# Optimization experiments

Measured on AMD Instinct MI355X. Metric: run time of the kernel, lower is better.

The kernel has to match this reference:

```python
import jax, jax.numpy as jnp
import numpy as np

B, S, D, H = 4, 1024, 1024, 16
DH = D // H  # head dim = 64
PAD = -1e7   # padding_num in source
EPS = 1e-3   # keras LayerNormalization default epsilon


def setup_inputs() -> dict:
    key = jax.random.key(0)
    ks = jax.random.split(key, 8)
    return {
        "queries": jax.random.normal(ks[0], (B, S, D), jnp.float32),
        "keys": jax.random.normal(ks[1], (B, S, D), jnp.float32),
        "values": jax.random.normal(ks[2], (B, S, D), jnp.float32),
        "query_masks": jax.random.randint(ks[3], (B, S), 0, 2, jnp.int32),
        "key_masks": jax.random.randint(ks[4], (B, S), 0, 2, jnp.int32),
        "Wq": jax.random.normal(ks[5], (D, D), jnp.float32) * (D ** -0.5),
        "Wk": jax.random.normal(ks[6], (D, D), jnp.float32) * (D ** -0.5),
        "Wv": jax.random.normal(ks[7], (D, D), jnp.float32) * (D ** -0.5),
        "gamma": jnp.ones((D,), jnp.float32),
        "beta": jnp.zeros((D,), jnp.float32),
    }


def reference(queries, keys, values, query_masks, key_masks, Wq, Wk, Wv, gamma, beta):
    # QKV projections (no bias)
    Q = queries @ Wq  # [B,S,D]
    K = keys @ Wk
    V = values @ Wv
    # split heads: tf.split(axis=2)+concat(axis=0) == head-major layout [H,B,S,DH]
    Qh = Q.reshape(B, S, H, DH).transpose(2, 0, 1, 3)
    Kh = K.reshape(B, S, H, DH).transpose(2, 0, 1, 3)
    Vh = V.reshape(B, S, H, DH).transpose(2, 0, 1, 3)
    # scaled scores; note source scales by head_dim ** 0.5 (d_k of split K)
    scores = jnp.einsum("hbqd,hbkd->hbqk", Qh, Kh) / (DH ** 0.5)
    # additive key mask: positions where key_mask==0 get large negative
    scores = jnp.where(key_masks[None, :, None, :] == 0, PAD, scores)
    attn = jax.nn.softmax(scores, axis=-1)
    # multiplicative query mask AFTER softmax (as in source)
    attn = attn * query_masks[None, :, :, None].astype(jnp.float32)
    out = jnp.einsum("hbqk,hbkd->hbqd", attn, Vh)  # [H,B,S,DH]
    # merge heads back: concat over feature axis in head order
    out = out.transpose(1, 2, 0, 3).reshape(B, S, D)
    # residual + LayerNorm
    res = queries + out
    mean = jnp.mean(res, axis=-1, keepdims=True)
    var = jnp.mean(jnp.square(res - mean), axis=-1, keepdims=True)
    return gamma * (res - mean) * jax.lax.rsqrt(var + EPS) + beta
```

## Files before the change

### kernel.cpp

```cpp
#include <hip/hip_runtime.h>

#define BB   4
#define SS   1024
#define DD   1024
#define HH   16
#define DHH  64
#define LN_EPS  (1e-3f)
#define NTT  ((size_t)BB * SS * DD)

typedef unsigned short u16;
typedef __attribute__((ext_vector_type(8))) short bf16x8;
typedef __attribute__((ext_vector_type(4))) float f32x4;

__device__ __forceinline__ u16 f2bf(float f) {
    union { float f; unsigned int u; } v; v.f = f;
    return (u16)((v.u + 0x7FFFu + ((v.u >> 16) & 1u)) >> 16);
}

__device__ __forceinline__ void cp16(void* lds, const void* g) {
    __builtin_amdgcn_global_load_lds(
        (const __attribute__((address_space(1))) unsigned int*)g,
        (__attribute__((address_space(3))) unsigned int*)lds, 16, 0, 0);
}


__device__ __forceinline__ void phase_conv(const float* __restrict__ q,
                                           const float* __restrict__ k,
                                           const float* __restrict__ v,
                                           u16* __restrict__ Abf,
                                           int gtid, int nthr) {
    const int total = (int)(3 * NTT / 8);
    for (int i = gtid; i < total; i += nthr) {
        const float* s = (i < 524288) ? q : (i < 1048576) ? k : v;
        const int off = i & 524287;
        const float4 f0 = ((const float4*)s)[off * 2];
        const float4 f1 = ((const float4*)s)[off * 2 + 1];
        union { u16 u[8]; uint4 o; } t;
        t.u[0] = f2bf(f0.x); t.u[1] = f2bf(f0.y);
        t.u[2] = f2bf(f0.z); t.u[3] = f2bf(f0.w);
        t.u[4] = f2bf(f1.x); t.u[5] = f2bf(f1.y);
        t.u[6] = f2bf(f1.z); t.u[7] = f2bf(f1.w);
        ((uint4*)Abf)[i] = t.o;
    }
}

__device__ __forceinline__ void phase_wtile(float (*Ts)[65], int vb,
                                            const float* __restrict__ Wq,
                                            const float* __restrict__ Wk,
                                            const float* __restrict__ Wv,
                                            u16* __restrict__ WtA) {
    const int tid = threadIdx.x;
    const float* W = (vb < 256) ? Wq : (vb < 512) ? Wk : Wv;
    u16* Wt = WtA + (size_t)(vb >> 8) * DD * DD;
    const int idx = vb & 255;
    const int k0 = (idx >> 4) * 64, n0 = (idx & 15) * 64;
    #pragma unroll
    for (int it = 0; it < 4; ++it) {
        const int i2 = tid + it * 256;
        const int r = i2 >> 4, c4 = (i2 & 15) * 4;
        const float4 vv = *(const float4*)&W[(size_t)(k0 + r) * DD + n0 + c4];
        Ts[r][c4 + 0] = vv.x; Ts[r][c4 + 1] = vv.y;
        Ts[r][c4 + 2] = vv.z; Ts[r][c4 + 3] = vv.w;
    }
    __syncthreads();
    const int n = tid >> 2, kc = (tid & 3) * 16;
    #pragma unroll
    for (int p = 0; p < 8; ++p) {
        const unsigned int lo = f2bf(Ts[kc + p * 2 + 0][n]);
        const unsigned int hi = f2bf(Ts[kc + p * 2 + 1][n]);
        *(unsigned int*)&Wt[(size_t)(n0 + n) * DD + k0 + kc + p * 2] = lo | (hi << 16);
    }
}

template <int NJ>
__device__ __forceinline__ void gemm_tile(u16* __restrict__ smem,
                                          const u16* __restrict__ A,
                                          const u16* __restrict__ B,
                                          int m0, int n0, int z,
                                          u16* __restrict__ Qbf,
                                          u16* __restrict__ Kbf,
                                          u16* __restrict__ Vtb) {
    u16* As = smem;
    u16* Bs = smem + 8192;
    const int tid  = threadIdx.x;
    const int wave = tid >> 6, lane = tid & 63;
    const int ln = lane & 15, quad = lane >> 4;
    const int mw = (wave & 1) * 64, nw = (wave >> 1) * (NJ * 16);

    f32x4 acc[4][NJ];
    #pragma unroll
    for (int i = 0; i < 4; ++i)
        #pragma unroll
        for (int j = 0; j < NJ; ++j) acc[i][j] = (f32x4){0.f, 0.f, 0.f, 0.f};

    for (int k0 = 0; k0 < DD; k0 += 64) {
        __syncthreads();
        #pragma unroll
        for (int w = 0; w < 4; ++w) {
            const int s = w * 256 + wave * 64 + lane;
            const int r = s >> 3, csrc = (s & 7) ^ (r & 7);
            cp16(&As[(size_t)(w * 256 + wave * 64) * 8],
                 &A[(size_t)(m0 + r) * DD + k0 + csrc * 8]);
        }
        #pragma unroll
        for (int w = 0; w < NJ; ++w) {
            const int s = w * 256 + wave * 64 + lane;
            const int r = s >> 3, csrc = (s & 7) ^ (r & 7);
            cp16(&Bs[(size_t)(w * 256 + wave * 64) * 8],
                 &B[(size_t)(n0 + r) * DD + k0 + csrc * 8]);
        }
        __syncthreads();

        #pragma unroll
        for (int kk = 0; kk < 2; ++kk) {
            bf16x8 af[4], bfv[NJ];
            #pragma unroll
            for (int i = 0; i < 4; ++i) {
                const int r = mw + i * 16 + ln;
                af[i] = *(const bf16x8*)&As[((r << 3) + ((kk * 4 + quad) ^ (r & 7))) << 3];
            }
            #pragma unroll
            for (int j = 0; j < NJ; ++j) {
                const int r = nw + j * 16 + ln;
                bfv[j] = *(const bf16x8*)&Bs[((r << 3) + ((kk * 4 + quad) ^ (r & 7))) << 3];
            }
            #pragma unroll
            for (int i = 0; i < 4; ++i)
                #pragma unroll
                for (int j = 0; j < NJ; ++j)
                    acc[i][j] = __builtin_amdgcn_mfma_f32_16x16x32_bf16(af[i], bfv[j], acc[i][j], 0, 0, 0);
        }
    }

    if (z < 2) {
        u16* C = (z == 0) ? Qbf : Kbf;
        const float scale = (z == 0) ? 0.125f : 1.0f;
        #pragma unroll
        for (int i = 0; i < 4; ++i) {
            const int mbase = m0 + mw + i * 16 + quad * 4;
            const int bb = mbase >> 10, sb = mbase & 1023;
            #pragma unroll
            for (int j = 0; j < NJ; ++j) {
                const int n = n0 + nw + j * 16 + ln;
                const int hh = n >> 6, dh = n & 63;
                #pragma unroll
                for (int r = 0; r < 4; ++r)
                    C[(((size_t)bb * HH + hh) * SS + sb + r) * DHH + dh] =
                        f2bf(acc[i][j][r] * scale);
            }
        }
    } else {
        #pragma unroll
        for (int i = 0; i < 4; ++i) {
            const int mbase = m0 + mw + i * 16 + quad * 4;
            const int bb = mbase >> 10, sb = mbase & 1023;
            #pragma unroll
            for (int j = 0; j < NJ; ++j) {
                const int n = n0 + nw + j * 16 + ln;
                const int hh = n >> 6, dh = n & 63;
                uint2 pk;
                pk.x = (unsigned int)f2bf(acc[i][j][0]) | ((unsigned int)f2bf(acc[i][j][1]) << 16);
                pk.y = (unsigned int)f2bf(acc[i][j][2]) | ((unsigned int)f2bf(acc[i][j][3]) << 16);
                *(uint2*)&Vtb[(((size_t)bb * HH + hh) * DHH + dh) * SS + sb] = pk;
            }
        }
    }
}

__device__ __forceinline__ void phase_gemm(u16* __restrict__ smem, int vb,
                                           const u16* __restrict__ Abf,
                                           const u16* __restrict__ WtA,
                                           u16* __restrict__ Qbf,
                                           u16* __restrict__ Kbf,
                                           u16* __restrict__ Vtb) {
    const int z = (vb < 256) ? 0 : (vb < 512) ? 1 : 2;
    const int xcd = vb & 7;
    const u16* A = Abf + (size_t)z * NTT;
    const u16* B = WtA + (size_t)z * DD * DD;
    if (z < 2) {
        const int t = (vb & 255) >> 3;
        gemm_tile<4>(smem, A, B, (xcd * 4 + (t & 3)) * 128, (t >> 2) * 128,
                     z, Qbf, Kbf, Vtb);
    } else {
        const int t = (vb - 512) >> 3;
        gemm_tile<2>(smem, A, B, (xcd * 4 + (t & 3)) * 128, (t >> 2) * 64,
                     z, Qbf, Kbf, Vtb);
    }
}

__device__ __forceinline__ void phase_attn(u16* __restrict__ smem, int vb,
                                           const u16* __restrict__ Qbf,
                                           const u16* __restrict__ Kbf,
                                           const u16* __restrict__ Vtb,
                                           const int* __restrict__ qmask,
                                           const int* __restrict__ kmask,
                                           float* __restrict__ Ob) {
    u16* QPs = smem;
    u16* Ks  = smem + 4352;
    u16* Vs  = smem + 8448;
    const int tid  = threadIdx.x;
    const int wave = tid >> 6, lane = tid & 63;
    const int ln = lane & 15, quad = lane >> 4;
    const int xcd  = vb & 7;
    const int rest = vb >> 3;
    const int bh   = (rest & 7) * 8 + xcd;
    const int qt   = rest >> 3;
    const int b    = bh >> 4, h = bh & 15;
    const int q0   = qt * 64;
    const size_t bhs = (size_t)b * HH + h;

    #pragma unroll
    for (int w = 0; w < 2; ++w) {
        const int s = w * 256 + wave * 64 + lane;
        const int r = s >> 3, csrc = (s & 7) ^ (r & 7);
        cp16(&QPs[(size_t)(w * 256 + wave * 64) * 8],
             &Qbf[(bhs * SS + q0 + r) * DHH + csrc * 8]);
    }
    __syncthreads();

    bf16x8 qf[2];
    #pragma unroll
    for (int kk = 0; kk < 2; ++kk) {
        const int r = wave * 16 + ln;
        qf[kk] = *(const bf16x8*)&QPs[((r << 3) + ((kk * 4 + quad) ^ (r & 7))) << 3];
    }

    f32x4 o[4] = {};
    float lsum[4] = {0.f, 0.f, 0.f, 0.f};
    const f32x4 zero = {0.f, 0.f, 0.f, 0.f};

    for (int kt = 0; kt < SS / 64; ++kt) {
        __syncthreads();
        #pragma unroll
        for (int w = 0; w < 2; ++w) {
            const int s = w * 256 + wave * 64 + lane;
            const int r = s >> 3, csrc = (s & 7) ^ (r & 7);
            cp16(&Ks[(size_t)(w * 256 + wave * 64) * 8],
                 &Kbf[(bhs * SS + kt * 64 + r) * DHH + csrc * 8]);
            cp16(&Vs[(size_t)(w * 256 + wave * 64) * 8],
                 &Vtb[(bhs * DHH + r) * SS + kt * 64 + csrc * 8]);
        }
        __syncthreads();

        #pragma unroll
        for (int nt = 0; nt < 4; ++nt) {
            const int krow = nt * 16 + ln;
            const bf16x8 k0f = *(const bf16x8*)&Ks[((krow << 3) + ((0 + quad) ^ (krow & 7))) << 3];
            const bf16x8 k1f = *(const bf16x8*)&Ks[((krow << 3) + ((4 + quad) ^ (krow & 7))) << 3];
            f32x4 sacc = __builtin_amdgcn_mfma_f32_16x16x32_bf16(qf[0], k0f, zero, 0, 0, 0);
            sacc = __builtin_amdgcn_mfma_f32_16x16x32_bf16(qf[1], k1f, sacc, 0, 0, 0);
            const int km = kmask[b * SS + kt * 64 + krow];
            #pragma unroll
            for (int r = 0; r < 4; ++r) {
                const float p = km ? __expf(sacc[r]) : 0.0f;
                lsum[r] += p;
                QPs[(wave * 16 + quad * 4 + r) * 68 + nt * 16 + ln] = f2bf(p);
            }
        }

        #pragma unroll
        for (int kk2 = 0; kk2 < 2; ++kk2) {
            const bf16x8 pf = *(const bf16x8*)&QPs[(wave * 16 + ln) * 68 + kk2 * 32 + quad * 8];
            #pragma unroll
            for (int nt2 = 0; nt2 < 4; ++nt2) {
                const int vrow = nt2 * 16 + ln;
                const bf16x8 vf = *(const bf16x8*)&Vs[((vrow << 3) + ((kk2 * 4 + quad) ^ (vrow & 7))) << 3];
                o[nt2] = __builtin_amdgcn_mfma_f32_16x16x32_bf16(pf, vf, o[nt2], 0, 0, 0);
            }
        }
    }

    #pragma unroll
    for (int r = 0; r < 4; ++r) {
        #pragma unroll
        for (int off = 1; off < 16; off <<= 1)
            lsum[r] += __shfl_xor(lsum[r], off);
        const int qq = q0 + wave * 16 + quad * 4 + r;
        const float scale = (float)qmask[b * SS + qq] / lsum[r];
        #pragma unroll
        for (int nt2 = 0; nt2 < 4; ++nt2)
            Ob[((size_t)b * SS + qq) * DD + h * DHH + nt2 * 16 + ln] = o[nt2][r] * scale;
    }
}

__device__ __forceinline__ void phase_ln(int row, float* __restrict__ sred,
                                         const float* __restrict__ q,
                                         const float* __restrict__ Ob,
                                         const float* __restrict__ gamma,
                                         const float* __restrict__ beta,
                                         float* __restrict__ out) {
    const int tid = threadIdx.x;
    const int wid = tid >> 6, lane = tid & 63;
    const float4 qv = ((const float4*)q)[(size_t)row * 256 + tid];
    const float4 av = ((const float4*)Ob)[(size_t)row * 256 + tid];
    float4 vv;
    vv.x = qv.x + av.x; vv.y = qv.y + av.y;
    vv.z = qv.z + av.z; vv.w = qv.w + av.w;

    float sum = vv.x + vv.y + vv.z + vv.w;
    #pragma unroll
    for (int off = 32; off; off >>= 1) sum += __shfl_down(sum, off);
    if (lane == 0) sred[wid] = sum;
    __syncthreads();
    const float mean = (sred[0] + sred[1] + sred[2] + sred[3]) * (1.0f / DD);
    __syncthreads();

    const float dx = vv.x - mean, dy = vv.y - mean;
    const float dz = vv.z - mean, dw = vv.w - mean;
    float vs = dx * dx + dy * dy + dz * dz + dw * dw;
    #pragma unroll
    for (int off = 32; off; off >>= 1) vs += __shfl_down(vs, off);
    if (lane == 0) sred[wid] = vs;
    __syncthreads();
    const float var = (sred[0] + sred[1] + sred[2] + sred[3]) * (1.0f / DD);
    const float inv = rsqrtf(var + LN_EPS);

    const float4 g  = ((const float4*)gamma)[tid];
    const float4 bt = ((const float4*)beta)[tid];
    float4 ov;
    ov.x = g.x * dx * inv + bt.x; ov.y = g.y * dy * inv + bt.y;
    ov.z = g.z * dz * inv + bt.z; ov.w = g.w * dw * inv + bt.w;
    ((float4*)out)[(size_t)row * 256 + tid] = ov;
    __syncthreads();
}

__global__ __launch_bounds__(256) void k_prep(
    const float* __restrict__ q, const float* __restrict__ k,
    const float* __restrict__ v,
    const float* __restrict__ Wq, const float* __restrict__ Wk,
    const float* __restrict__ Wv,
    u16* __restrict__ Abf, u16* __restrict__ WtA) {
    __shared__ float Ts[64][65];
    if (blockIdx.x < 768) phase_wtile(Ts, blockIdx.x, Wq, Wk, Wv, WtA);
    phase_conv(q, k, v, Abf, blockIdx.x * 256 + threadIdx.x, gridDim.x * 256);
}

__global__ __launch_bounds__(256, 4) void k_gemm(
    const u16* __restrict__ Abf, const u16* __restrict__ WtA,
    u16* __restrict__ Qbf, u16* __restrict__ Kbf, u16* __restrict__ Vtb) {
    __shared__ __align__(16) u16 smem[16384];
    phase_gemm(smem, blockIdx.x, Abf, WtA, Qbf, Kbf, Vtb);
}

__global__ __launch_bounds__(256, 4) void k_attn(
    const u16* __restrict__ Qbf, const u16* __restrict__ Kbf,
    const u16* __restrict__ Vtb,
    const int* __restrict__ qmask, const int* __restrict__ kmask,
    float* __restrict__ Ob) {
    __shared__ __align__(16) u16 smem[12544];
    phase_attn(smem, blockIdx.x, Qbf, Kbf, Vtb, qmask, kmask, Ob);
}

__global__ __launch_bounds__(256) void k_ln(
    const float* __restrict__ q, const float* __restrict__ Ob,
    const float* __restrict__ gamma, const float* __restrict__ beta,
    float* __restrict__ out) {
    __shared__ float sred[4];
    #pragma unroll
    for (int rr = 0; rr < 4; ++rr)
        phase_ln(blockIdx.x * 4 + rr, sred, q, Ob, gamma, beta, out);
}

extern "C" void kernel_launch(void* const* d_in, const int* in_sizes, int n_in,
                              void* d_out, int out_size, void* d_ws, size_t ws_size,
                              hipStream_t stream) {
    const float* queries = (const float*)d_in[0];
    const float* keys    = (const float*)d_in[1];
    const float* values  = (const float*)d_in[2];
    const int*   qmask   = (const int*)d_in[3];
    const int*   kmask   = (const int*)d_in[4];
    const float* Wq      = (const float*)d_in[5];
    const float* Wk      = (const float*)d_in[6];
    const float* Wv      = (const float*)d_in[7];
    const float* gamma   = (const float*)d_in[8];
    const float* beta    = (const float*)d_in[9];
    float* out = (float*)d_out;
    u16* ws = (u16*)d_ws;

    u16*   Abf = ws;
    float* Ob  = (float*)ws;
    u16*   Qbf = ws + 3 * NTT;
    u16*   Kbf = Qbf + NTT;
    u16*   Vtb = Kbf + NTT;
    u16*   WtA = Vtb + NTT;

    k_prep<<<1024, 256, 0, stream>>>(queries, keys, values, Wq, Wk, Wv, Abf, WtA);
    k_gemm<<<1024, 256, 0, stream>>>(Abf, WtA, Qbf, Kbf, Vtb);
    k_attn<<<1024, 256, 0, stream>>>(Qbf, Kbf, Vtb, qmask, kmask, Ob);
    k_ln<<<1024, 256, 0, stream>>>(queries, Ob, gamma, beta, out);
}
```

Baseline: 207.4 us.

## Fuse fp32-to-bf16 conversion into GEMM loads and merge LayerNorm into attention

Drops the separate activation conversion pass. The GEMM now reads fp32 q/k/v directly, converts to bf16 in registers and stores to LDS, replacing the async global-to-LDS copy. Weight transposition moves into the GEMM kernel behind a grid-wide atomic flag barrier, and LayerNorm is folded into the attention kernel using per-row-group counters that wait for all 16 heads. This removes two launches and the bf16 activation round trip through memory. The cost is spin-wait barriers that depend on all 1024 blocks being co-resident, which risks deadlock, plus an extra memset and synchronous fp32 loads in the GEMM loop.

```diff
diff --git a/kernel.cpp b/kernel.cpp
--- a/kernel.cpp
+++ b/kernel.cpp
@@ -21,27 +21,6 @@
     __builtin_amdgcn_global_load_lds(
         (const __attribute__((address_space(1))) unsigned int*)g,
         (__attribute__((address_space(3))) unsigned int*)lds, 16, 0, 0);
-}
-
-
-__device__ __forceinline__ void phase_conv(const float* __restrict__ q,
-                                           const float* __restrict__ k,
-                                           const float* __restrict__ v,
-                                           u16* __restrict__ Abf,
-                                           int gtid, int nthr) {
-    const int total = (int)(3 * NTT / 8);
-    for (int i = gtid; i < total; i += nthr) {
-        const float* s = (i < 524288) ? q : (i < 1048576) ? k : v;
-        const int off = i & 524287;
-        const float4 f0 = ((const float4*)s)[off * 2];
-        const float4 f1 = ((const float4*)s)[off * 2 + 1];
-        union { u16 u[8]; uint4 o; } t;
-        t.u[0] = f2bf(f0.x); t.u[1] = f2bf(f0.y);
-        t.u[2] = f2bf(f0.z); t.u[3] = f2bf(f0.w);
-        t.u[4] = f2bf(f1.x); t.u[5] = f2bf(f1.y);
-        t.u[6] = f2bf(f1.z); t.u[7] = f2bf(f1.w);
-        ((uint4*)Abf)[i] = t.o;
-    }
 }
 
 __device__ __forceinline__ void phase_wtile(float (*Ts)[65], int vb,
@@ -74,7 +53,7 @@
 
 template <int NJ>
 __device__ __forceinline__ void gemm_tile(u16* __restrict__ smem,
-                                          const u16* __restrict__ A,
+                                          const float* __restrict__ A,
                                           const u16* __restrict__ B,
                                           int m0, int n0, int z,
                                           u16* __restrict__ Qbf,
@@ -97,10 +76,16 @@
         __syncthreads();
         #pragma unroll
         for (int w = 0; w < 4; ++w) {
-            const int s = w * 256 + wave * 64 + lane;
+            const int s = w * 256 + tid;
             const int r = s >> 3, csrc = (s & 7) ^ (r & 7);
-            cp16(&As[(size_t)(w * 256 + wave * 64) * 8],
-                 &A[(size_t)(m0 + r) * DD + k0 + csrc * 8]);
+            const float4 f0 = *(const float4*)&A[(size_t)(m0 + r) * DD + k0 + csrc * 8];
+            const float4 f1 = *(const float4*)&A[(size_t)(m0 + r) * DD + k0 + csrc * 8 + 4];
+            union { u16 u[8]; uint4 o; } t;
+            t.u[0] = f2bf(f0.x); t.u[1] = f2bf(f0.y);
+            t.u[2] = f2bf(f0.z); t.u[3] = f2bf(f0.w);
+            t.u[4] = f2bf(f1.x); t.u[5] = f2bf(f1.y);
+            t.u[6] = f2bf(f1.z); t.u[7] = f2bf(f1.w);
+            *(uint4*)&As[(size_t)s * 8] = t.o;
         }
         #pragma unroll
         for (int w = 0; w < NJ; ++w) {
@@ -164,27 +149,6 @@
                 *(uint2*)&Vtb[(((size_t)bb * HH + hh) * DHH + dh) * SS + sb] = pk;
             }
         }
-    }
-}
-
-__device__ __forceinline__ void phase_gemm(u16* __restrict__ smem, int vb,
-                                           const u16* __restrict__ Abf,
-                                           const u16* __restrict__ WtA,
-                                           u16* __restrict__ Qbf,
-                                           u16* __restrict__ Kbf,
-                                           u16* __restrict__ Vtb) {
-    const int z = (vb < 256) ? 0 : (vb < 512) ? 1 : 2;
-    const int xcd = vb & 7;
-    const u16* A = Abf + (size_t)z * NTT;
-    const u16* B = WtA + (size_t)z * DD * DD;
-    if (z < 2) {
-        const int t = (vb & 255) >> 3;
-        gemm_tile<4>(smem, A, B, (xcd * 4 + (t & 3)) * 128, (t >> 2) * 128,
-                     z, Qbf, Kbf, Vtb);
-    } else {
-        const int t = (vb - 512) >> 3;
-        gemm_tile<2>(smem, A, B, (xcd * 4 + (t & 3)) * 128, (t >> 2) * 64,
-                     z, Qbf, Kbf, Vtb);
     }
 }
 
@@ -324,41 +288,77 @@
     __syncthreads();
 }
 
-__global__ __launch_bounds__(256) void k_prep(
+__global__ __launch_bounds__(256, 4) void k_gemm(
     const float* __restrict__ q, const float* __restrict__ k,
     const float* __restrict__ v,
     const float* __restrict__ Wq, const float* __restrict__ Wk,
     const float* __restrict__ Wv,
-    u16* __restrict__ Abf, u16* __restrict__ WtA) {
-    __shared__ float Ts[64][65];
-    if (blockIdx.x < 768) phase_wtile(Ts, blockIdx.x, Wq, Wk, Wv, WtA);
-    phase_conv(q, k, v, Abf, blockIdx.x * 256 + threadIdx.x, gridDim.x * 256);
-}
-
-__global__ __launch_bounds__(256, 4) void k_gemm(
-    const u16* __restrict__ Abf, const u16* __restrict__ WtA,
-    u16* __restrict__ Qbf, u16* __restrict__ Kbf, u16* __restrict__ Vtb) {
+    u16* __restrict__ WtA, u16* __restrict__ Qbf, u16* __restrict__ Kbf,
+    u16* __restrict__ Vtb, int* __restrict__ flag) {
     __shared__ __align__(16) u16 smem[16384];
-    phase_gemm(smem, blockIdx.x, Abf, WtA, Qbf, Kbf, Vtb);
+    const int bid = blockIdx.x, tid = threadIdx.x;
+
+    if (bid < 768)
+        phase_wtile((float (*)[65])smem, bid, Wq, Wk, Wv, WtA);
+    __syncthreads();
+    if (tid == 0) {
+        if (bid < 768) {
+            __threadfence();
+            __hip_atomic_fetch_add(flag, 1, __ATOMIC_ACQ_REL, __HIP_MEMORY_SCOPE_AGENT);
+        }
+        while (__hip_atomic_load(flag, __ATOMIC_ACQUIRE, __HIP_MEMORY_SCOPE_AGENT) < 768) {}
+        __threadfence();
+    }
+    __syncthreads();
+
+    const int z = (bid < 256) ? 0 : (bid < 512) ? 1 : 2;
+    const int xcd = bid & 7;
+    const float* A = (z == 0) ? q : (z == 1) ? k : v;
+    const u16* B = WtA + (size_t)z * DD * DD;
+    if (z < 2) {
+        const int t = (bid & 255) >> 3;
+        gemm_tile<4>(smem, A, B, (xcd * 4 + (t & 3)) * 128, (t >> 2) * 128,
+                     z, Qbf, Kbf, Vtb);
+    } else {
+        const int t = (bid - 512) >> 3;
+        gemm_tile<2>(smem, A, B, (xcd * 4 + (t & 3)) * 128, (t >> 2) * 64,
+                     z, Qbf, Kbf, Vtb);
+    }
 }
 
 __global__ __launch_bounds__(256, 4) void k_attn(
     const u16* __restrict__ Qbf, const u16* __restrict__ Kbf,
     const u16* __restrict__ Vtb,
     const int* __restrict__ qmask, const int* __restrict__ kmask,
-    float* __restrict__ Ob) {
+    const float* __restrict__ q, const float* __restrict__ gamma,
+    const float* __restrict__ beta,
+    float* __restrict__ Ob, float* __restrict__ out, int* __restrict__ cnt) {
     __shared__ __align__(16) u16 smem[12544];
-    phase_attn(smem, blockIdx.x, Qbf, Kbf, Vtb, qmask, kmask, Ob);
-}
-
-__global__ __launch_bounds__(256) void k_ln(
-    const float* __restrict__ q, const float* __restrict__ Ob,
-    const float* __restrict__ gamma, const float* __restrict__ beta,
-    float* __restrict__ out) {
-    __shared__ float sred[4];
+    const int bid = blockIdx.x, tid = threadIdx.x;
+
+    phase_attn(smem, bid, Qbf, Kbf, Vtb, qmask, kmask, Ob);
+
+    const int xcd  = bid & 7;
+    const int rest = bid >> 3;
+    const int bh   = (rest & 7) * 8 + xcd;
+    const int qt   = rest >> 3;
+    const int b    = bh >> 4, h = bh & 15;
+    const int gi   = b * 16 + qt;
+
+    __syncthreads();
+    if (tid == 0) {
+        __threadfence();
+        __hip_atomic_fetch_add(&cnt[gi * 16], 1, __ATOMIC_ACQ_REL, __HIP_MEMORY_SCOPE_AGENT);
+        while (__hip_atomic_load(&cnt[gi * 16], __ATOMIC_ACQUIRE, __HIP_MEMORY_SCOPE_AGENT) < 16) {}
+        __threadfence();
+    }
+    __syncthreads();
+
+    float* sred = (float*)smem;
+    const int row0 = b * SS + qt * 64 + h * 4;
     #pragma unroll
     for (int rr = 0; rr < 4; ++rr)
-        phase_ln(blockIdx.x * 4 + rr, sred, q, Ob, gamma, beta, out);
+        phase_ln(row0 + rr, sred, q, Ob, gamma, beta, out);
 }
 
 extern "C" void kernel_launch(void* const* d_in, const int* in_sizes, int n_in,
@@ -377,15 +377,19 @@
     float* out = (float*)d_out;
     u16* ws = (u16*)d_ws;
 
-    u16*   Abf = ws;
     float* Ob  = (float*)ws;
-    u16*   Qbf = ws + 3 * NTT;
+    u16*   Qbf = ws + 2 * NTT;
     u16*   Kbf = Qbf + NTT;
     u16*   Vtb = Kbf + NTT;
     u16*   WtA = Vtb + NTT;
-
-    k_prep<<<1024, 256, 0, stream>>>(queries, keys, values, Wq, Wk, Wv, Abf, WtA);
-    k_gemm<<<1024, 256, 0, stream>>>(Abf, WtA, Qbf, Kbf, Vtb);
-    k_attn<<<1024, 256, 0, stream>>>(Qbf, Kbf, Vtb, qmask, kmask, Ob);
-    k_ln<<<1024, 256, 0, stream>>>(queries, Ob, gamma, beta, out);
-}
+    int*   flags = (int*)(WtA + 3 * (size_t)DD * DD);
+    int*   gflag = flags;
+    int*   cnt   = flags + 16;
+
+    (void)hipMemsetAsync(flags, 0, 8192, stream);
+
+    k_gemm<<<1024, 256, 0, stream>>>(queries, keys, values, Wq, Wk, Wv,
+                                     WtA, Qbf, Kbf, Vtb, gflag);
+    k_attn<<<1024, 256, 0, stream>>>(Qbf, Kbf, Vtb, qmask, kmask,
+                                     queries, gamma, beta, Ob, out, cnt);
+}
```

New measurement: 446.0 us. 115% more time.
